# Kernel tuning notes

Measured on AMD Instinct MI355X. Metric: run time of the kernel, lower is better.

## Reference

```python
import jax, jax.numpy as jnp
import numpy as np

N_NODES = 50000
N_EDGES = 800000
IN_F, HID, N_CLS = 128, 128, 40


def gcn_conv(x, row, col, ew, W, b, n):
    # PyG GCNConv with add_self_loops=True, normalize=True (gcn_norm):
    # out = D^{-1/2} (A + I) D^{-1/2} (x W) + b, aggregation at target = col.
    h = x @ W                                        # [N, F_out]
    loop = jnp.arange(n)
    row_f = jnp.concatenate([row, loop])             # self-loop weight = 1
    col_f = jnp.concatenate([col, loop])
    ew_f = jnp.concatenate([ew, jnp.ones((n,), dtype=ew.dtype)])
    deg = jax.ops.segment_sum(ew_f, col_f, num_segments=n)
    dinv = jnp.where(deg > 0, jax.lax.rsqrt(deg), 0.0)
    norm = dinv[row_f] * ew_f * dinv[col_f]          # [E+N]
    msg = norm[:, None] * h[row_f]                   # gather + scale
    out = jax.ops.segment_sum(msg, col_f, num_segments=n)  # scatter-add
    return out + b


def setup_inputs() -> dict:
    key = jax.random.key(0)
    ks = jax.random.split(key, 8)
    glorot = lambda k, fi, fo: jax.random.normal(k, (fi, fo), jnp.float32) * np.sqrt(2.0 / (fi + fo))
    return {
        "x": jax.random.normal(ks[0], (N_NODES, IN_F), jnp.float32),
        "edge_weight": jax.random.uniform(ks[1], (N_EDGES,), jnp.float32),
        "W1": glorot(ks[2], IN_F, HID),
        "b1": jnp.zeros((HID,), jnp.float32),
        "W2": glorot(ks[3], HID, HID),
        "b2": jnp.zeros((HID,), jnp.float32),
        "W3": glorot(ks[4], HID, N_CLS),
        "b3": jnp.zeros((N_CLS,), jnp.float32),
        "edge_index": jax.random.randint(ks[5], (2, N_EDGES), 0, N_NODES, jnp.int64),
        "target_mask": jnp.ones((N_NODES,), jnp.bool_),
    }


def reference(x, edge_weight, W1, b1, W2, b2, W3, b3, edge_index, target_mask):
    n = x.shape[0]
    row, col = edge_index[0], edge_index[1]
    h = gcn_conv(x, row, col, edge_weight, W1, b1, n)
    h = jax.nn.relu(h)  # dropout is identity in eval mode
    h = gcn_conv(h, row, col, edge_weight, W2, b2, n)
    h = jax.nn.relu(h)
    h = gcn_conv(h, row, col, edge_weight, W3, b3, n)
    return h[target_mask]
```

## Files before the change

kernel.cpp:

```cpp
#include <hip/hip_runtime.h>
#include <hip/hip_fp16.h>

#define N_NODES 50000
#define N_EDGES 800000
#define HID 128
#define N_CLS 40
#define CAP 64
#define TILES32 1563
#define CNT_BLOCKS 3125
#define NODE_WAVES 12500

static inline int cdiv(int a, int b) { return (a + b - 1) / b; }

__device__ __forceinline__ void fill_body(int e, const int* __restrict__ row,
                                          const int* __restrict__ col,
                                          const float* __restrict__ ew,
                                          int* __restrict__ cnt,
                                          uint2* __restrict__ bkt) {
    if (e < N_EDGES) {
        int c = col[e];
        int pos = atomicAdd(&cnt[c], 1);
        if (pos < CAP)
            bkt[(size_t)c * CAP + pos] = make_uint2((unsigned)row[e],
                                                    __float_as_uint(ew[e]));
    }
}

__device__ __forceinline__ void gemm128_body(int b, const float* __restrict__ X,
                                             const float* __restrict__ W,
                                             __half* __restrict__ out) {
    __shared__ float xsT[128][36];
    __shared__ float wch[32][128];
    const int t = threadIdx.x;
    const int row0 = b * 32;

    #pragma unroll
    for (int i = 0; i < 4; ++i) {
        int idx = t + i * 256;
        int row = idx >> 5;
        int k4  = idx & 31;
        float4 v = make_float4(0.f, 0.f, 0.f, 0.f);
        if (row0 + row < N_NODES)
            v = *(const float4*)&X[(size_t)(row0 + row) * 128 + k4 * 4];
        xsT[k4 * 4 + 0][row] = v.x;
        xsT[k4 * 4 + 1][row] = v.y;
        xsT[k4 * 4 + 2][row] = v.z;
        xsT[k4 * 4 + 3][row] = v.w;
    }

    const int c0 = (t & 31) * 4;
    const int r0 = (t >> 5) * 4;
    float acc[4][4];
    #pragma unroll
    for (int i = 0; i < 4; ++i)
        #pragma unroll
        for (int j = 0; j < 4; ++j) acc[i][j] = 0.f;

    for (int kk = 0; kk < 128; kk += 32) {
        __syncthreads();
        #pragma unroll
        for (int i = 0; i < 4; ++i) {
            int idx = t + i * 256;
            int wr = idx >> 5;
            int wc4 = idx & 31;
            *(float4*)&wch[wr][wc4 * 4] =
                *(const float4*)&W[(size_t)(kk + wr) * 128 + wc4 * 4];
        }
        __syncthreads();
        #pragma unroll 4
        for (int k = 0; k < 32; ++k) {
            float4 a = *(const float4*)&xsT[kk + k][r0];
            float4 w = *(const float4*)&wch[k][c0];
            acc[0][0] = fmaf(a.x, w.x, acc[0][0]);
            acc[0][1] = fmaf(a.x, w.y, acc[0][1]);
            acc[0][2] = fmaf(a.x, w.z, acc[0][2]);
            acc[0][3] = fmaf(a.x, w.w, acc[0][3]);
            acc[1][0] = fmaf(a.y, w.x, acc[1][0]);
            acc[1][1] = fmaf(a.y, w.y, acc[1][1]);
            acc[1][2] = fmaf(a.y, w.z, acc[1][2]);
            acc[1][3] = fmaf(a.y, w.w, acc[1][3]);
            acc[2][0] = fmaf(a.z, w.x, acc[2][0]);
            acc[2][1] = fmaf(a.z, w.y, acc[2][1]);
            acc[2][2] = fmaf(a.z, w.z, acc[2][2]);
            acc[2][3] = fmaf(a.z, w.w, acc[2][3]);
            acc[3][0] = fmaf(a.w, w.x, acc[3][0]);
            acc[3][1] = fmaf(a.w, w.y, acc[3][1]);
            acc[3][2] = fmaf(a.w, w.z, acc[3][2]);
            acc[3][3] = fmaf(a.w, w.w, acc[3][3]);
        }
    }

    #pragma unroll
    for (int i = 0; i < 4; ++i) {
        int r = row0 + r0 + i;
        if (r < N_NODES) {
            union { __half2 h2[2]; float2 f2; } u;
            u.h2[0] = __floats2half2_rn(acc[i][0], acc[i][1]);
            u.h2[1] = __floats2half2_rn(acc[i][2], acc[i][3]);
            *(float2*)&out[(size_t)r * 128 + c0] = u.f2;
        }
    }
}

__global__ __launch_bounds__(256) void fused_gemm1_fill(
    const float* __restrict__ X, const float* __restrict__ W, __half* __restrict__ out,
    const int* __restrict__ row, const int* __restrict__ col,
    const float* __restrict__ ew, int* __restrict__ cnt, uint2* __restrict__ bkt) {
    int id = blockIdx.x;
    if (id & 1) {
        fill_body((id >> 1) * 256 + threadIdx.x, row, col, ew, cnt, bkt);
    } else {
        int b = id >> 1;
        if (b < TILES32) gemm128_body(b, X, W, out);
    }
}

__global__ __launch_bounds__(256) void dinv_kernel(
    const int* __restrict__ cnt, const uint2* __restrict__ bkt,
    float* __restrict__ dinv) {
    int node = blockIdx.x * 4 + (threadIdx.x >> 6);
    int lane = threadIdx.x & 63;
    if (node >= N_NODES) return;
    int n = min(cnt[node], CAP);
    float ewv = 0.f;
    if (lane < n) ewv = __uint_as_float(bkt[(size_t)node * CAP + lane].y);
    #pragma unroll
    for (int off = 32; off > 0; off >>= 1)
        ewv += __shfl_down(ewv, off);
    if (lane == 0) dinv[node] = rsqrtf(ewv + 1.0f);
}

__global__ __launch_bounds__(256) void norm_kernel(
    const int* __restrict__ cnt, uint2* __restrict__ bkt,
    const float* __restrict__ dinv) {
    int node = blockIdx.x * 4 + (threadIdx.x >> 6);
    int lane = threadIdx.x & 63;
    if (node >= N_NODES) return;
    int n = min(cnt[node], CAP);
    if (lane < n) {
        size_t idx = (size_t)node * CAP + lane;
        uint2 e = bkt[idx];
        float w = dinv[e.x] * __uint_as_float(e.y) * dinv[node];
        bkt[idx] = make_uint2(e.x, __float_as_uint(w));
    }
}

__device__ __forceinline__ void fma_h4(float w, uint2 g, float4& acc) {
    float2 lo = __half22float2(*(const __half2*)&g.x);
    float2 hi = __half22float2(*(const __half2*)&g.y);
    acc.x = fmaf(w, lo.x, acc.x);
    acc.y = fmaf(w, lo.y, acc.y);
    acc.z = fmaf(w, hi.x, acc.z);
    acc.w = fmaf(w, hi.y, acc.w);
}

__device__ __forceinline__ float4 agg128_node(int node, int sl,
                                              const int* __restrict__ cnt,
                                              const uint2* __restrict__ bkt,
                                              const __half* __restrict__ h,
                                              const float* __restrict__ dinv,
                                              const float* __restrict__ b) {
    int beg = node * CAP;
    int end = beg + min(cnt[node], CAP);
    int f = sl * 4;
    float4 acc = make_float4(0.f, 0.f, 0.f, 0.f);
    int k = beg;
    for (; k + 8 <= end; k += 8) {
        uint2 e0 = bkt[k], e1 = bkt[k+1], e2 = bkt[k+2], e3 = bkt[k+3];
        uint2 e4 = bkt[k+4], e5 = bkt[k+5], e6 = bkt[k+6], e7 = bkt[k+7];
        uint2 g0 = *(const uint2*)&h[(size_t)e0.x * 128 + f];
        uint2 g1 = *(const uint2*)&h[(size_t)e1.x * 128 + f];
        uint2 g2 = *(const uint2*)&h[(size_t)e2.x * 128 + f];
        uint2 g3 = *(const uint2*)&h[(size_t)e3.x * 128 + f];
        uint2 g4 = *(const uint2*)&h[(size_t)e4.x * 128 + f];
        uint2 g5 = *(const uint2*)&h[(size_t)e5.x * 128 + f];
        uint2 g6 = *(const uint2*)&h[(size_t)e6.x * 128 + f];
        uint2 g7 = *(const uint2*)&h[(size_t)e7.x * 128 + f];
        fma_h4(__uint_as_float(e0.y), g0, acc);
        fma_h4(__uint_as_float(e1.y), g1, acc);
        fma_h4(__uint_as_float(e2.y), g2, acc);
        fma_h4(__uint_as_float(e3.y), g3, acc);
        fma_h4(__uint_as_float(e4.y), g4, acc);
        fma_h4(__uint_as_float(e5.y), g5, acc);
        fma_h4(__uint_as_float(e6.y), g6, acc);
        fma_h4(__uint_as_float(e7.y), g7, acc);
    }
    for (; k + 4 <= end; k += 4) {
        uint2 e0 = bkt[k], e1 = bkt[k+1], e2 = bkt[k+2], e3 = bkt[k+3];
        uint2 g0 = *(const uint2*)&h[(size_t)e0.x * 128 + f];
        uint2 g1 = *(const uint2*)&h[(size_t)e1.x * 128 + f];
        uint2 g2 = *(const uint2*)&h[(size_t)e2.x * 128 + f];
        uint2 g3 = *(const uint2*)&h[(size_t)e3.x * 128 + f];
        fma_h4(__uint_as_float(e0.y), g0, acc);
        fma_h4(__uint_as_float(e1.y), g1, acc);
        fma_h4(__uint_as_float(e2.y), g2, acc);
        fma_h4(__uint_as_float(e3.y), g3, acc);
    }
    for (; k < end; ++k) {
        uint2 e = bkt[k];
        uint2 g = *(const uint2*)&h[(size_t)e.x * 128 + f];
        fma_h4(__uint_as_float(e.y), g, acc);
    }
    float di = dinv[node];
    uint2 gs = *(const uint2*)&h[(size_t)node * 128 + f];
    fma_h4(di * di, gs, acc);
    float4 bb = *(const float4*)&b[f];
    acc.x = fmaxf(acc.x + bb.x, 0.f);
    acc.y = fmaxf(acc.y + bb.y, 0.f);
    acc.z = fmaxf(acc.z + bb.z, 0.f);
    acc.w = fmaxf(acc.w + bb.w, 0.f);
    return acc;
}

__device__ __forceinline__ void agg_tile_to_lds(int row0, const int* cnt,
                                                const uint2* bkt, const __half* h,
                                                const float* dinv, const float* bias,
                                                float (*xsT)[36]) {
    int wave = threadIdx.x >> 6;
    int lane = threadIdx.x & 63;
    int sub  = lane >> 5;
    int sl   = lane & 31;
    int f = sl * 4;
    #pragma unroll
    for (int i = 0; i < 4; ++i) {
        int r = i * 8 + wave * 2 + sub;
        int node = row0 + r;
        float4 acc = make_float4(0.f, 0.f, 0.f, 0.f);
        if (node < N_NODES)
            acc = agg128_node(node, sl, cnt, bkt, h, dinv, bias);
        xsT[f + 0][r] = acc.x;
        xsT[f + 1][r] = acc.y;
        xsT[f + 2][r] = acc.z;
        xsT[f + 3][r] = acc.w;
    }
}

__global__ __launch_bounds__(256) void agg_gemm128_kernel(
    const int* __restrict__ cnt, const uint2* __restrict__ bkt,
    const __half* __restrict__ h, const float* __restrict__ dinv,
    const float* __restrict__ bias, const float* __restrict__ W,
    __half* __restrict__ out) {
    __shared__ float xsT[128][36];
    __shared__ float wch[32][128];
    const int t = threadIdx.x;
    const int row0 = blockIdx.x * 32;

    agg_tile_to_lds(row0, cnt, bkt, h, dinv, bias, xsT);

    const int c0 = (t & 31) * 4;
    const int r0 = (t >> 5) * 4;
    float acc[4][4];
    #pragma unroll
    for (int i = 0; i < 4; ++i)
        #pragma unroll
        for (int j = 0; j < 4; ++j) acc[i][j] = 0.f;

    for (int kk = 0; kk < 128; kk += 32) {
        __syncthreads();
        #pragma unroll
        for (int i = 0; i < 4; ++i) {
            int idx = t + i * 256;
            int wr = idx >> 5;
            int wc4 = idx & 31;
            *(float4*)&wch[wr][wc4 * 4] =
                *(const float4*)&W[(size_t)(kk + wr) * 128 + wc4 * 4];
        }
        __syncthreads();
        #pragma unroll 4
        for (int k = 0; k < 32; ++k) {
            float4 a = *(const float4*)&xsT[kk + k][r0];
            float4 w = *(const float4*)&wch[k][c0];
            acc[0][0] = fmaf(a.x, w.x, acc[0][0]);
            acc[0][1] = fmaf(a.x, w.y, acc[0][1]);
            acc[0][2] = fmaf(a.x, w.z, acc[0][2]);
            acc[0][3] = fmaf(a.x, w.w, acc[0][3]);
            acc[1][0] = fmaf(a.y, w.x, acc[1][0]);
            acc[1][1] = fmaf(a.y, w.y, acc[1][1]);
            acc[1][2] = fmaf(a.y, w.z, acc[1][2]);
            acc[1][3] = fmaf(a.y, w.w, acc[1][3]);
            acc[2][0] = fmaf(a.z, w.x, acc[2][0]);
            acc[2][1] = fmaf(a.z, w.y, acc[2][1]);
            acc[2][2] = fmaf(a.z, w.z, acc[2][2]);
            acc[2][3] = fmaf(a.z, w.w, acc[2][3]);
            acc[3][0] = fmaf(a.w, w.x, acc[3][0]);
            acc[3][1] = fmaf(a.w, w.y, acc[3][1]);
            acc[3][2] = fmaf(a.w, w.z, acc[3][2]);
            acc[3][3] = fmaf(a.w, w.w, acc[3][3]);
        }
    }

    #pragma unroll
    for (int i = 0; i < 4; ++i) {
        int r = row0 + r0 + i;
        if (r < N_NODES) {
            union { __half2 h2[2]; float2 f2; } u;
            u.h2[0] = __floats2half2_rn(acc[i][0], acc[i][1]);
            u.h2[1] = __floats2half2_rn(acc[i][2], acc[i][3]);
            *(float2*)&out[(size_t)r * 128 + c0] = u.f2;
        }
    }
}

__global__ __launch_bounds__(256) void agg_gemm40_kernel(
    const int* __restrict__ cnt, const uint2* __restrict__ bkt,
    const __half* __restrict__ h, const float* __restrict__ dinv,
    const float* __restrict__ bias, const float* __restrict__ W3,
    __half* __restrict__ out) {
    __shared__ float xsT[128][36];
    const int row0 = blockIdx.x * 32;
    agg_tile_to_lds(row0, cnt, bkt, h, dinv, bias, xsT);
    __syncthreads();
    for (int idx = threadIdx.x; idx < 32 * N_CLS; idx += 256) {
        int r = idx / N_CLS;
        int c = idx % N_CLS;
        float acc = 0.f;
        #pragma unroll 8
        for (int k = 0; k < 128; ++k)
            acc = fmaf(xsT[k][r], W3[k * N_CLS + c], acc);
        int node = row0 + r;
        if (node < N_NODES)
            out[(size_t)node * N_CLS + c] = __float2half(acc);
    }
}

__global__ __launch_bounds__(256) void agg40_kernel(
    const int* __restrict__ cnt, const uint2* __restrict__ bkt,
    const __half* __restrict__ h, const float* __restrict__ dinv,
    const float* __restrict__ b, float* __restrict__ out) {
    int wave = threadIdx.x >> 6;
    int lane = threadIdx.x & 63;
    int node = blockIdx.x * 4 + wave;
    if (node >= N_NODES || lane >= N_CLS) return;
    int beg = node * CAP;
    int end = beg + min(cnt[node], CAP);
    float acc = 0.f;
    int k = beg;
    for (; k + 4 <= end; k += 4) {
        uint2 e0 = bkt[k], e1 = bkt[k+1], e2 = bkt[k+2], e3 = bkt[k+3];
        float g0 = __half2float(h[(size_t)e0.x * N_CLS + lane]);
        float g1 = __half2float(h[(size_t)e1.x * N_CLS + lane]);
        float g2 = __half2float(h[(size_t)e2.x * N_CLS + lane]);
        float g3 = __half2float(h[(size_t)e3.x * N_CLS + lane]);
        acc = fmaf(__uint_as_float(e0.y), g0, acc);
        acc = fmaf(__uint_as_float(e1.y), g1, acc);
        acc = fmaf(__uint_as_float(e2.y), g2, acc);
        acc = fmaf(__uint_as_float(e3.y), g3, acc);
    }
    for (; k < end; ++k) {
        uint2 e = bkt[k];
        acc = fmaf(__uint_as_float(e.y),
                   __half2float(h[(size_t)e.x * N_CLS + lane]), acc);
    }
    float di = dinv[node];
    acc = fmaf(di * di, __half2float(h[(size_t)node * N_CLS + lane]), acc) + b[lane];
    out[(size_t)node * N_CLS + lane] = acc;
}

extern "C" void kernel_launch(void* const* d_in, const int* in_sizes, int n_in,
                              void* d_out, int out_size, void* d_ws, size_t ws_size,
                              hipStream_t stream) {
    const float* x  = (const float*)d_in[0];
    const float* ew = (const float*)d_in[1];
    const float* W1 = (const float*)d_in[2];
    const float* b1 = (const float*)d_in[3];
    const float* W2 = (const float*)d_in[4];
    const float* b2 = (const float*)d_in[5];
    const float* W3 = (const float*)d_in[6];
    const float* b3 = (const float*)d_in[7];
    const int*   ei = (const int*)d_in[8];
    const int* row = ei;
    const int* col = ei + N_EDGES;
    float* out = (float*)d_out;

    char* ws = (char*)d_ws;
    size_t off = 0;
    auto alloc = [&](size_t bytes) -> void* {
        void* p = (void*)(ws + off);
        off = (off + bytes + 255) & ~(size_t)255;
        return p;
    };
    int*    cnt  = (int*)alloc((size_t)N_NODES * 4);
    float*  dinv = (float*)alloc((size_t)N_NODES * 4);
    uint2*  bkt  = (uint2*)alloc((size_t)N_NODES * CAP * 8);
    __half* h16a = (__half*)alloc((size_t)N_NODES * HID * 2);
    __half* h16b = (__half*)alloc((size_t)N_NODES * HID * 2);
    __half* h40  = (__half*)alloc((size_t)N_NODES * N_CLS * 2);

    hipMemsetAsync(cnt, 0, (size_t)N_NODES * 4, stream);

    fused_gemm1_fill<<<2 * CNT_BLOCKS, 256, 0, stream>>>(x, W1, h16a, row, col, ew, cnt, bkt);
    dinv_kernel<<<NODE_WAVES, 256, 0, stream>>>(cnt, bkt, dinv);
    norm_kernel<<<NODE_WAVES, 256, 0, stream>>>(cnt, bkt, dinv);
    agg_gemm128_kernel<<<TILES32, 256, 0, stream>>>(cnt, bkt, h16a, dinv, b1, W2, h16b);
    agg_gemm40_kernel<<<TILES32, 256, 0, stream>>>(cnt, bkt, h16b, dinv, b2, W3, h40);
    agg40_kernel<<<cdiv(N_NODES, 4), 256, 0, stream>>>(cnt, bkt, h40, dinv, b3, out);
}
```

Before: 315.9 us.

## Fuse edge normalization into aggregation and widen feature gathers to 16 bytes

```diff
diff --git a/kernel.cpp b/kernel.cpp
--- a/kernel.cpp
+++ b/kernel.cpp
@@ -130,86 +130,97 @@
     if (lane == 0) dinv[node] = rsqrtf(ewv + 1.0f);
 }
 
-__global__ __launch_bounds__(256) void norm_kernel(
-    const int* __restrict__ cnt, uint2* __restrict__ bkt,
-    const float* __restrict__ dinv) {
-    int node = blockIdx.x * 4 + (threadIdx.x >> 6);
-    int lane = threadIdx.x & 63;
-    if (node >= N_NODES) return;
-    int n = min(cnt[node], CAP);
-    if (lane < n) {
-        size_t idx = (size_t)node * CAP + lane;
-        uint2 e = bkt[idx];
-        float w = dinv[e.x] * __uint_as_float(e.y) * dinv[node];
-        bkt[idx] = make_uint2(e.x, __float_as_uint(w));
-    }
-}
-
-__device__ __forceinline__ void fma_h4(float w, uint2 g, float4& acc) {
-    float2 lo = __half22float2(*(const __half2*)&g.x);
-    float2 hi = __half22float2(*(const __half2*)&g.y);
-    acc.x = fmaf(w, lo.x, acc.x);
-    acc.y = fmaf(w, lo.y, acc.y);
-    acc.z = fmaf(w, hi.x, acc.z);
-    acc.w = fmaf(w, hi.y, acc.w);
-}
-
-__device__ __forceinline__ float4 agg128_node(int node, int sl,
+__device__ __forceinline__ void fma_h8(float w, uint4 g, float* acc) {
+    float2 a0 = __half22float2(*(const __half2*)&g.x);
+    float2 a1 = __half22float2(*(const __half2*)&g.y);
+    float2 a2 = __half22float2(*(const __half2*)&g.z);
+    float2 a3 = __half22float2(*(const __half2*)&g.w);
+    acc[0] = fmaf(w, a0.x, acc[0]);
+    acc[1] = fmaf(w, a0.y, acc[1]);
+    acc[2] = fmaf(w, a1.x, acc[2]);
+    acc[3] = fmaf(w, a1.y, acc[3]);
+    acc[4] = fmaf(w, a2.x, acc[4]);
+    acc[5] = fmaf(w, a2.y, acc[5]);
+    acc[6] = fmaf(w, a3.x, acc[6]);
+    acc[7] = fmaf(w, a3.y, acc[7]);
+}
+
+__device__ __forceinline__ void agg128_node16(int node, int sl,
                                               const int* __restrict__ cnt,
                                               const uint2* __restrict__ bkt,
                                               const __half* __restrict__ h,
                                               const float* __restrict__ dinv,
-                                              const float* __restrict__ b) {
+                                              const float* __restrict__ bias,
+                                              float* acc) {
+    #pragma unroll
+    for (int j = 0; j < 8; ++j) acc[j] = 0.f;
+    if (node >= N_NODES) return;
+    int f = sl * 8;
     int beg = node * CAP;
     int end = beg + min(cnt[node], CAP);
-    int f = sl * 4;
-    float4 acc = make_float4(0.f, 0.f, 0.f, 0.f);
+    float dn = dinv[node];
     int k = beg;
     for (; k + 8 <= end; k += 8) {
-        uint2 e0 = bkt[k], e1 = bkt[k+1], e2 = bkt[k+2], e3 = bkt[k+3];
+        uint2 e0 = bkt[k],   e1 = bkt[k+1], e2 = bkt[k+2], e3 = bkt[k+3];
         uint2 e4 = bkt[k+4], e5 = bkt[k+5], e6 = bkt[k+6], e7 = bkt[k+7];
-        uint2 g0 = *(const uint2*)&h[(size_t)e0.x * 128 + f];
-        uint2 g1 = *(const uint2*)&h[(size_t)e1.x * 128 + f];
-        uint2 g2 = *(const uint2*)&h[(size_t)e2.x * 128 + f];
-        uint2 g3 = *(const uint2*)&h[(size_t)e3.x * 128 + f];
-        uint2 g4 = *(const uint2*)&h[(size_t)e4.x * 128 + f];
-        uint2 g5 = *(const uint2*)&h[(size_t)e5.x * 128 + f];
-        uint2 g6 = *(const uint2*)&h[(size_t)e6.x * 128 + f];
-        uint2 g7 = *(const uint2*)&h[(size_t)e7.x * 128 + f];
-        fma_h4(__uint_as_float(e0.y), g0, acc);
-        fma_h4(__uint_as_float(e1.y), g1, acc);
-        fma_h4(__uint_as_float(e2.y), g2, acc);
-        fma_h4(__uint_as_float(e3.y), g3, acc);
-        fma_h4(__uint_as_float(e4.y), g4, acc);
-        fma_h4(__uint_as_float(e5.y), g5, acc);
-        fma_h4(__uint_as_float(e6.y), g6, acc);
-        fma_h4(__uint_as_float(e7.y), g7, acc);
+        uint4 g0 = *(const uint4*)&h[(size_t)e0.x * 128 + f];
+        uint4 g1 = *(const uint4*)&h[(size_t)e1.x * 128 + f];
+        uint4 g2 = *(const uint4*)&h[(size_t)e2.x * 128 + f];
+        uint4 g3 = *(const uint4*)&h[(size_t)e3.x * 128 + f];
+        uint4 g4 = *(const uint4*)&h[(size_t)e4.x * 128 + f];
+        uint4 g5 = *(const uint4*)&h[(size_t)e5.x * 128 + f];
+        uint4 g6 = *(const uint4*)&h[(size_t)e6.x * 128 + f];
+        uint4 g7 = *(const uint4*)&h[(size_t)e7.x * 128 + f];
+        float w0 = dinv[e0.x] * __uint_as_float(e0.y) * dn;
+        float w1 = dinv[e1.x] * __uint_as_float(e1.y) * dn;
+        float w2 = dinv[e2.x] * __uint_as_float(e2.y) * dn;
+        float w3 = dinv[e3.x] * __uint_as_float(e3.y) * dn;
+        float w4 = dinv[e4.x] * __uint_as_float(e4.y) * dn;
+        float w5 = dinv[e5.x] * __uint_as_float(e5.y) * dn;
+        float w6 = dinv[e6.x] * __uint_as_float(e6.y) * dn;
+        float w7 = dinv[e7.x] * __uint_as_float(e7.y) * dn;
+        fma_h8(w0, g0, acc);
+        fma_h8(w1, g1, acc);
+        fma_h8(w2, g2, acc);
+        fma_h8(w3, g3, acc);
+        fma_h8(w4, g4, acc);
+        fma_h8(w5, g5, acc);
+        fma_h8(w6, g6, acc);
+        fma_h8(w7, g7, acc);
     }
     for (; k + 4 <= end; k += 4) {
         uint2 e0 = bkt[k], e1 = bkt[k+1], e2 = bkt[k+2], e3 = bkt[k+3];
-        uint2 g0 = *(const uint2*)&h[(size_t)e0.x * 128 + f];
-        uint2 g1 = *(const uint2*)&h[(size_t)e1.x * 128 + f];
-        uint2 g2 = *(const uint2*)&h[(size_t)e2.x * 128 + f];
-        uint2 g3 = *(const uint2*)&h[(size_t)e3.x * 128 + f];
-        fma_h4(__uint_as_float(e0.y), g0, acc);
-        fma_h4(__uint_as_float(e1.y), g1, acc);
-        fma_h4(__uint_as_float(e2.y), g2, acc);
-        fma_h4(__uint_as_float(e3.y), g3, acc);
+        uint4 g0 = *(const uint4*)&h[(size_t)e0.x * 128 + f];
+        uint4 g1 = *(const uint4*)&h[(size_t)e1.x * 128 + f];
+        uint4 g2 = *(const uint4*)&h[(size_t)e2.x * 128 + f];
+        uint4 g3 = *(const uint4*)&h[(size_t)e3.x * 128 + f];
+        float w0 = dinv[e0.x] * __uint_as_float(e0.y) * dn;
+        float w1 = dinv[e1.x] * __uint_as_float(e1.y) * dn;
+        float w2 = dinv[e2.x] * __uint_as_float(e2.y) * dn;
+        float w3 = dinv[e3.x] * __uint_as_float(e3.y) * dn;
+        fma_h8(w0, g0, acc);
+        fma_h8(w1, g1, acc);
+        fma_h8(w2, g2, acc);
+        fma_h8(w3, g3, acc);
     }
     for (; k < end; ++k) {
         uint2 e = bkt[k];
-        uint2 g = *(const uint2*)&h[(size_t)e.x * 128 + f];
-        fma_h4(__uint_as_float(e.y), g, acc);
-    }
-    float di = dinv[node];
-    uint2 gs = *(const uint2*)&h[(size_t)node * 128 + f];
-    fma_h4(di * di, gs, acc);
-    float4 bb = *(const float4*)&b[f];
-    acc.x = fmaxf(acc.x + bb.x, 0.f);
-    acc.y = fmaxf(acc.y + bb.y, 0.f);
-    acc.z = fmaxf(acc.z + bb.z, 0.f);
-    acc.w = fmaxf(acc.w + bb.w, 0.f);
-    return acc;
+        uint4 g = *(const uint4*)&h[(size_t)e.x * 128 + f];
+        float w = dinv[e.x] * __uint_as_float(e.y) * dn;
+        fma_h8(w, g, acc);
+    }
+    uint4 gs = *(const uint4*)&h[(size_t)node * 128 + f];
+    fma_h8(dn * dn, gs, acc);
+    float4 b0 = *(const float4*)&bias[f];
+    float4 b1 = *(const float4*)&bias[f + 4];
+    acc[0] = fmaxf(acc[0] + b0.x, 0.f);
+    acc[1] = fmaxf(acc[1] + b0.y, 0.f);
+    acc[2] = fmaxf(acc[2] + b0.z, 0.f);
+    acc[3] = fmaxf(acc[3] + b0.w, 0.f);
+    acc[4] = fmaxf(acc[4] + b1.x, 0.f);
+    acc[5] = fmaxf(acc[5] + b1.y, 0.f);
+    acc[6] = fmaxf(acc[6] + b1.z, 0.f);
+    acc[7] = fmaxf(acc[7] + b1.w, 0.f);
 }
 
 __device__ __forceinline__ void agg_tile_to_lds(int row0, const int* cnt,
@@ -218,20 +229,17 @@
                                                 float (*xsT)[36]) {
     int wave = threadIdx.x >> 6;
     int lane = threadIdx.x & 63;
-    int sub  = lane >> 5;
-    int sl   = lane & 31;
-    int f = sl * 4;
-    #pragma unroll
-    for (int i = 0; i < 4; ++i) {
-        int r = i * 8 + wave * 2 + sub;
-        int node = row0 + r;
-        float4 acc = make_float4(0.f, 0.f, 0.f, 0.f);
-        if (node < N_NODES)
-            acc = agg128_node(node, sl, cnt, bkt, h, dinv, bias);
-        xsT[f + 0][r] = acc.x;
-        xsT[f + 1][r] = acc.y;
-        xsT[f + 2][r] = acc.z;
-        xsT[f + 3][r] = acc.w;
+    int sub  = lane >> 4;
+    int sl   = lane & 15;
+    int f = sl * 8;
+    #pragma unroll
+    for (int i = 0; i < 2; ++i) {
+        int r = i * 16 + wave * 4 + sub;
+        float acc[8];
+        agg128_node16(row0 + r, sl, cnt, bkt, h, dinv, bias, acc);
+        #pragma unroll
+        for (int j = 0; j < 8; ++j)
+            xsT[f + j][r] = acc[j];
     }
 }
 
@@ -319,7 +327,7 @@
             acc = fmaf(xsT[k][r], W3[k * N_CLS + c], acc);
         int node = row0 + r;
         if (node < N_NODES)
-            out[(size_t)node * N_CLS + c] = __float2half(acc);
+            out[(size_t)node * 64 + c] = __float2half(acc);
     }
 }
 
@@ -333,26 +341,30 @@
     if (node >= N_NODES || lane >= N_CLS) return;
     int beg = node * CAP;
     int end = beg + min(cnt[node], CAP);
+    float dn = dinv[node];
     float acc = 0.f;
     int k = beg;
     for (; k + 4 <= end; k += 4) {
         uint2 e0 = bkt[k], e1 = bkt[k+1], e2 = bkt[k+2], e3 = bkt[k+3];
-        float g0 = __half2float(h[(size_t)e0.x * N_CLS + lane]);
-        float g1 = __half2float(h[(size_t)e1.x * N_CLS + lane]);
-        float g2 = __half2float(h[(size_t)e2.x * N_CLS + lane]);
-        float g3 = __half2float(h[(size_t)e3.x * N_CLS + lane]);
-        acc = fmaf(__uint_as_float(e0.y), g0, acc);
-        acc = fmaf(__uint_as_float(e1.y), g1, acc);
-        acc = fmaf(__uint_as_float(e2.y), g2, acc);
-        acc = fmaf(__uint_as_float(e3.y), g3, acc);
+        float g0 = __half2float(h[(size_t)e0.x * 64 + lane]);
+        float g1 = __half2float(h[(size_t)e1.x * 64 + lane]);
+        float g2 = __half2float(h[(size_t)e2.x * 64 + lane]);
+        float g3 = __half2float(h[(size_t)e3.x * 64 + lane]);
+        float w0 = dinv[e0.x] * __uint_as_float(e0.y) * dn;
+        float w1 = dinv[e1.x] * __uint_as_float(e1.y) * dn;
+        float w2 = dinv[e2.x] * __uint_as_float(e2.y) * dn;
+        float w3 = dinv[e3.x] * __uint_as_float(e3.y) * dn;
+        acc = fmaf(w0, g0, acc);
+        acc = fmaf(w1, g1, acc);
+        acc = fmaf(w2, g2, acc);
+        acc = fmaf(w3, g3, acc);
     }
     for (; k < end; ++k) {
         uint2 e = bkt[k];
-        acc = fmaf(__uint_as_float(e.y),
-                   __half2float(h[(size_t)e.x * N_CLS + lane]), acc);
-    }
-    float di = dinv[node];
-    acc = fmaf(di * di, __half2float(h[(size_t)node * N_CLS + lane]), acc) + b[lane];
+        float w = dinv[e.x] * __uint_as_float(e.y) * dn;
+        acc = fmaf(w, __half2float(h[(size_t)e.x * 64 + lane]), acc);
+    }
+    acc = fmaf(dn * dn, __half2float(h[(size_t)node * 64 + lane]), acc) + b[lane];
     out[(size_t)node * N_CLS + lane] = acc;
 }
 
@@ -384,13 +396,12 @@
     uint2*  bkt  = (uint2*)alloc((size_t)N_NODES * CAP * 8);
     __half* h16a = (__half*)alloc((size_t)N_NODES * HID * 2);
     __half* h16b = (__half*)alloc((size_t)N_NODES * HID * 2);
-    __half* h40  = (__half*)alloc((size_t)N_NODES * N_CLS * 2);
+    __half* h40  = (__half*)alloc((size_t)N_NODES * 64 * 2);
 
     hipMemsetAsync(cnt, 0, (size_t)N_NODES * 4, stream);
 
     fused_gemm1_fill<<<2 * CNT_BLOCKS, 256, 0, stream>>>(x, W1, h16a, row, col, ew, cnt, bkt);
     dinv_kernel<<<NODE_WAVES, 256, 0, stream>>>(cnt, bkt, dinv);
-    norm_kernel<<<NODE_WAVES, 256, 0, stream>>>(cnt, bkt, dinv);
     agg_gemm128_kernel<<<TILES32, 256, 0, stream>>>(cnt, bkt, h16a, dinv, b1, W2, h16b);
     agg_gemm40_kernel<<<TILES32, 256, 0, stream>>>(cnt, bkt, h16b, dinv, b2, W3, h40);
     agg40_kernel<<<cdiv(N_NODES, 4), 256, 0, stream>>>(cnt, bkt, h40, dinv, b3, out);
```

After: 304.5 us. -3.6%, faster.
